# Optimization experiments

Hardware: AMD Instinct MI355X
Metric: run time of the kernel (lower is better)

## Reference

```python
import jax, jax.numpy as jnp
import numpy as np

B, S, DIM = 8, 1024, 192
D2 = 2 * DIM            # inner width 384
CH = 4                  # cell heads (= qk_size)
HD = D2 // CH           # 96 head dim
NB = D2 // 4            # 96 block-diagonal blocks
BLK = D2 // NB          # block size 4
TAU = float(HD) ** 0.5


def setup_inputs() -> dict:
    key = jax.random.key(0)
    ks = jax.random.split(key, 16)
    r = lambda i, shp, s=0.02: jax.random.normal(ks[i], shp, jnp.float32) * s
    return {
        "x": jax.random.normal(ks[0], (B, S, DIM), jnp.float32),
        "ln_g": jnp.ones((DIM,), jnp.float32), "ln_b": jnp.zeros((DIM,), jnp.float32),
        "w1": r(1, (D2, DIM)), "b1": jnp.zeros((D2,), jnp.float32),
        "w2": r(2, (D2, DIM)), "b2": jnp.zeros((D2,), jnp.float32),
        "conv_w": r(3, (D2, 1, 3), 0.1), "conv_b": jnp.zeros((D2,), jnp.float32),
        "qw": r(4, (NB, BLK, BLK), 0.1), "qb": jnp.zeros((D2,), jnp.float32),
        "kw": r(5, (NB, BLK, BLK), 0.1), "kb": jnp.zeros((D2,), jnp.float32),
        "vw": r(6, (NB, BLK, BLK), 0.1), "vb": jnp.zeros((D2,), jnp.float32),
        "wi": r(7, (CH, 3 * D2)), "bi": jax.random.normal(ks[8], (CH,), jnp.float32) * 0.1,
        "wf": r(9, (CH, 3 * D2)), "bf": jnp.linspace(3.0, 6.0, CH).astype(jnp.float32),
        "gn_g": jnp.ones((D2,), jnp.float32), "gn_b": jnp.zeros((D2,), jnp.float32),
        "wo": r(10, (DIM, D2)), "bo": jnp.zeros((DIM,), jnp.float32),
        "skip": jnp.ones((D2,), jnp.float32),
    }


def _layernorm(x, g, b):
    m = x.mean(-1, keepdims=True)
    v = ((x - m) ** 2).mean(-1, keepdims=True)
    return (x - m) / jnp.sqrt(v + 1e-5) * g + b


def _blockdiag(x, w, b):
    # x: [B,S,D2] -> blocks [B,S,NB,BLK]; w: [NB, out_blk, in_blk]
    bs, sq, _ = x.shape
    y = jnp.einsum('bsni,noi->bsno', x.reshape(bs, sq, NB, BLK), w)
    return y.reshape(bs, sq, D2) + b


def _dwconv(x, w, b):
    # depthwise conv over sequence: x [B,S,C] -> [B,C,S] conv -> [B,S,C]
    y = jax.lax.conv_general_dilated(
        x.transpose(0, 2, 1), w, window_strides=(1,), padding=[(1, 1)],
        dimension_numbers=('NCH', 'OIH', 'NCH'), feature_group_count=D2)
    return y.transpose(0, 2, 1) + b


def _cell(q, k, v, wi, bi, wf, bf, gn_g, gn_b):
    bs, sq, _ = q.shape
    gi = jnp.concatenate([q, k, v], axis=-1)                      # [B,S,3*D2]
    it = jnp.einsum('bsc,hc->bhs', gi, wi) + bi[None, :, None]    # [B,H,S]
    ft = jnp.einsum('bsc,hc->bhs', gi, wf) + bf[None, :, None]
    c = jnp.cumsum(jax.nn.log_sigmoid(ft), axis=-1)               # [B,H,S]
    logm = c[..., :, None] - c[..., None, :]                      # cum[i]-cum[j]
    mask = jnp.tril(jnp.ones((sq, sq), dtype=bool))
    f_act = jnp.where(mask, logm, -jnp.inf)
    dt = f_act + it[:, :, None, :]                                # add itilde over cols
    max_d = jnp.max(dt, axis=-1, keepdims=True)
    dmat = jnp.exp(dt - max_d)                                    # [B,H,S,S]
    qh = q.reshape(bs, sq, CH, HD).transpose(0, 2, 1, 3)
    kh = k.reshape(bs, sq, CH, HD).transpose(0, 2, 1, 3)
    vh = v.reshape(bs, sq, CH, HD).transpose(0, 2, 1, 3)
    ct = jnp.einsum('bhid,bhjd->bhij', qh, kh) * dmat / TAU
    maxit = jnp.maximum(jnp.abs(ct.sum(-1, keepdims=True)), jnp.exp(-max_d))
    h = jnp.einsum('bhij,bhjd->bhid', ct, vh) / (maxit + 1e-6)
    h = h.transpose(0, 2, 1, 3).reshape(bs, sq, CH, HD)           # per-token GroupNorm
    mu = h.mean(-1, keepdims=True)
    var = ((h - mu) ** 2).mean(-1, keepdims=True)
    h = (h - mu) / jnp.sqrt(var + 1e-5)
    h = h * gn_g.reshape(CH, HD) + gn_b.reshape(CH, HD)
    return h.reshape(bs, sq, D2)


def reference(x, ln_g, ln_b, w1, b1, w2, b2, conv_w, conv_b, qw, qb, kw, kb,
              vw, vb, wi, bi, wf, bf, gn_g, gn_b, wo, bo, skip):
    inputs = _layernorm(x, ln_g, ln_b)
    a = inputs @ w1.T + b1                   # [B,S,D2]
    bgate = jax.nn.silu(inputs @ w2.T + b2)  # [B,S,D2]
    qk = jax.nn.silu(_dwconv(a, conv_w, conv_b))
    q = _blockdiag(qk, qw, qb)
    k = _blockdiag(qk, kw, kb)
    v = _blockdiag(a, vw, vb)
    out1 = _cell(q, k, v, wi, bi, wf, bf, gn_g, gn_b)
    out1 = (out1 + skip * qk) * bgate
    out = out1 @ wo.T + bo
    return out + x
```

## Files before the change

kernel.cpp:

```cpp
#include <hip/hip_runtime.h>
#include <cstdint>

#define TAU_ 9.797958971132712f

typedef __attribute__((ext_vector_type(4))) float f32x4;
typedef __attribute__((ext_vector_type(8))) short short8;

#define DEV static __device__ __forceinline__

DEV unsigned short f2bf(float f){
  union { float f; unsigned u; } v; v.f = f;
  unsigned r = v.u + 0x7FFFu + ((v.u >> 16) & 1u);
  return (unsigned short)(r >> 16);
}
DEV unsigned pack2bf(float a, float b){
  unsigned r;
  asm("v_cvt_pk_bf16_f32 %0, %1, %2" : "=v"(r) : "v"(a), "v"(b));
  return r;
}
DEV float siluf_(float x){ return x / (1.f + __expf(-x)); }
DEV float logsigf_(float x){ return fminf(x, 0.f) - log1pf(__expf(-fabsf(x))); }

__global__ __launch_bounds__(256) void k01_prep(
    const float* __restrict__ x, const float* __restrict__ ln_g, const float* __restrict__ ln_b,
    const float* __restrict__ w1, const float* __restrict__ w2, const float* __restrict__ wo,
    short* __restrict__ xnbf, short* __restrict__ w12bf, short* __restrict__ wobf)
{
  const int tid = threadIdx.x;
  if(blockIdx.x >= 512){
    int idx = (blockIdx.x - 512) * 256 + tid;
    if(idx < 73728)       w12bf[idx] = (short)f2bf(w1[idx]);
    else if(idx < 147456) w12bf[idx] = (short)f2bf(w2[idx - 73728]);
    else                  wobf[idx - 147456] = (short)f2bf(wo[idx - 147456]);
    return;
  }
  const int t = blockIdx.x * 16 + (tid >> 4);
  const int g = tid & 15;
  const float* xr = x + (long)t * 192 + g * 12;
  f32x4 v0 = *(const f32x4*)(xr);
  f32x4 v1 = *(const f32x4*)(xr + 4);
  f32x4 v2 = *(const f32x4*)(xr + 8);
  float s  = v0[0]+v0[1]+v0[2]+v0[3] + v1[0]+v1[1]+v1[2]+v1[3] + v2[0]+v2[1]+v2[2]+v2[3];
  float sq = v0[0]*v0[0]+v0[1]*v0[1]+v0[2]*v0[2]+v0[3]*v0[3]
           + v1[0]*v1[0]+v1[1]*v1[1]+v1[2]*v1[2]+v1[3]*v1[3]
           + v2[0]*v2[0]+v2[1]*v2[1]+v2[2]*v2[2]+v2[3]*v2[3];
  s  += __shfl_xor(s, 1);  s  += __shfl_xor(s, 2);  s  += __shfl_xor(s, 4);  s  += __shfl_xor(s, 8);
  sq += __shfl_xor(sq, 1); sq += __shfl_xor(sq, 2); sq += __shfl_xor(sq, 4); sq += __shfl_xor(sq, 8);
  const float mean = s * (1.f/192.f);
  const float rstd = rsqrtf(sq * (1.f/192.f) - mean * mean + 1e-5f);
  const int c0 = g * 12;
  f32x4 g0 = *(const f32x4*)(ln_g + c0),     b0 = *(const f32x4*)(ln_b + c0);
  f32x4 g1 = *(const f32x4*)(ln_g + c0 + 4), b1 = *(const f32x4*)(ln_b + c0 + 4);
  f32x4 g2 = *(const f32x4*)(ln_g + c0 + 8), b2 = *(const f32x4*)(ln_b + c0 + 8);
  unsigned pk[6];
  pk[0] = pack2bf((v0[0]-mean)*rstd*g0[0]+b0[0], (v0[1]-mean)*rstd*g0[1]+b0[1]);
  pk[1] = pack2bf((v0[2]-mean)*rstd*g0[2]+b0[2], (v0[3]-mean)*rstd*g0[3]+b0[3]);
  pk[2] = pack2bf((v1[0]-mean)*rstd*g1[0]+b1[0], (v1[1]-mean)*rstd*g1[1]+b1[1]);
  pk[3] = pack2bf((v1[2]-mean)*rstd*g1[2]+b1[2], (v1[3]-mean)*rstd*g1[3]+b1[3]);
  pk[4] = pack2bf((v2[0]-mean)*rstd*g2[0]+b2[0], (v2[1]-mean)*rstd*g2[1]+b2[1]);
  pk[5] = pack2bf((v2[2]-mean)*rstd*g2[2]+b2[2], (v2[3]-mean)*rstd*g2[3]+b2[3]);
  uint2* xo = (uint2*)(xnbf + (long)t * 192 + g * 12);
  xo[0] = make_uint2(pk[0], pk[1]);
  xo[1] = make_uint2(pk[2], pk[3]);
  xo[2] = make_uint2(pk[4], pk[5]);
}

__global__ __launch_bounds__(256) void k1b_gemm(
    const short* __restrict__ xnbf, const short* __restrict__ w12bf,
    const float* __restrict__ b1, const float* __restrict__ b2,
    float* __restrict__ a, float* __restrict__ bgate)
{
  __shared__ short wt[18432];
  const int tid = threadIdx.x;
  const int ntg = blockIdx.x & 7;
  const int t0 = (blockIdx.x >> 3) * 64;
  {
    const short* src = w12bf + (long)ntg * 96 * 192;
    #pragma unroll
    for(int i = 0; i < 9; i++){
      const int u = i * 256 + tid;
      const int row = u / 24;
      const int dst = (u * 16) ^ ((row & 7) << 4);
      *(short8*)((char*)wt + dst) = *(const short8*)(src + u * 8);
    }
  }
  __syncthreads();
  const int widx = tid >> 6, lane = tid & 63, qg = lane >> 4, l16 = lane & 15;
  f32x4 acc[6];
  #pragma unroll
  for(int nt = 0; nt < 6; nt++) acc[nt] = (f32x4){0.f,0.f,0.f,0.f};
  const short* xrow = xnbf + (long)(t0 + widx * 16 + l16) * 192;
  #pragma unroll
  for(int kc = 0; kc < 6; kc++){
    short8 af = *(const short8*)(xrow + kc * 32 + 8 * qg);
    #pragma unroll
    for(int nt = 0; nt < 6; nt++){
      const int row = nt * 16 + l16;
      int byte = row * 384 + (kc * 32 + 8 * qg) * 2;
      byte ^= (row & 7) << 4;
      short8 bfr = *(const short8*)((const char*)wt + byte);
      acc[nt] = __builtin_amdgcn_mfma_f32_16x16x32_bf16(af, bfr, acc[nt], 0, 0, 0);
    }
  }
  const int half = ntg >> 2;
  float* dst = half ? bgate : a;
  const float* bias = half ? b2 : b1;
  const int ncol = (ntg & 3) * 96;
  #pragma unroll
  for(int nt = 0; nt < 6; nt++){
    const int n = ncol + nt * 16 + l16;
    const float bs = bias[n];
    #pragma unroll
    for(int r = 0; r < 4; r++){
      const int trow = t0 + widx * 16 + 4 * qg + r;
      float v = acc[nt][r] + bs;
      if(half) v = siluf_(v);
      dst[(long)trow * 384 + n] = v;
    }
  }
}

__global__ __launch_bounds__(256) void k2bv(
    const float* __restrict__ a, const float* __restrict__ cw, const float* __restrict__ cb,
    const float* __restrict__ qw, const float* __restrict__ qb,
    const float* __restrict__ kw, const float* __restrict__ kb,
    const float* __restrict__ vw, const float* __restrict__ vb,
    float* __restrict__ qkbuf, short* __restrict__ qbf, short* __restrict__ kbf,
    short* __restrict__ vtbf)
{
  __shared__ float vt[64][97];
  const int tid = threadIdx.x;
  const int bh = blockIdx.x >> 4;
  const int b = bh >> 2, h = bh & 3;
  const int s0 = (blockIdx.x & 15) << 6;
  #pragma unroll
  for(int it = 0; it < 6; it++){
    const int f = it * 256 + tid;
    const int sl = f / 24, c4l = f % 24;
    const int c4 = h * 24 + c4l;
    const int s = s0 + sl;
    const long t = (long)b * 1024 + s;
    const long abase = t * 384 + c4 * 4;
    f32x4 am = *(const f32x4*)(a + abase);
    f32x4 al = (s > 0)    ? *(const f32x4*)(a + abase - 384) : (f32x4){0.f,0.f,0.f,0.f};
    f32x4 ar = (s < 1023) ? *(const f32x4*)(a + abase + 384) : (f32x4){0.f,0.f,0.f,0.f};
    f32x4 cw0 = *(const f32x4*)(cw + c4 * 12);
    f32x4 cw1 = *(const f32x4*)(cw + c4 * 12 + 4);
    f32x4 cw2 = *(const f32x4*)(cw + c4 * 12 + 8);
    f32x4 cb4 = *(const f32x4*)(cb + c4 * 4);
    f32x4 in;
    in[0] = siluf_(cb4[0] + al[0]*cw0[0] + am[0]*cw0[1] + ar[0]*cw0[2]);
    in[1] = siluf_(cb4[1] + al[1]*cw0[3] + am[1]*cw1[0] + ar[1]*cw1[1]);
    in[2] = siluf_(cb4[2] + al[2]*cw1[2] + am[2]*cw1[3] + ar[2]*cw2[0]);
    in[3] = siluf_(cb4[3] + al[3]*cw2[1] + am[3]*cw2[2] + ar[3]*cw2[3]);
    *(f32x4*)(qkbuf + abase) = in;
    const long base = ((long)(b * 4 + h) * 1024 + s) * 96 + c4l * 4;
    {
      const float* w = qw + c4 * 16;
      float v0 = qb[c4*4+0] + w[0]*in[0]  + w[1]*in[1]  + w[2]*in[2]  + w[3]*in[3];
      float v1 = qb[c4*4+1] + w[4]*in[0]  + w[5]*in[1]  + w[6]*in[2]  + w[7]*in[3];
      float v2 = qb[c4*4+2] + w[8]*in[0]  + w[9]*in[1]  + w[10]*in[2] + w[11]*in[3];
      float v3 = qb[c4*4+3] + w[12]*in[0] + w[13]*in[1] + w[14]*in[2] + w[15]*in[3];
      uint2 pk; pk.x = pack2bf(v0, v1); pk.y = pack2bf(v2, v3);
      *(uint2*)(qbf + base) = pk;
    }
    {
      const float* w = kw + c4 * 16;
      float v0 = kb[c4*4+0] + w[0]*in[0]  + w[1]*in[1]  + w[2]*in[2]  + w[3]*in[3];
      float v1 = kb[c4*4+1] + w[4]*in[0]  + w[5]*in[1]  + w[6]*in[2]  + w[7]*in[3];
      float v2 = kb[c4*4+2] + w[8]*in[0]  + w[9]*in[1]  + w[10]*in[2] + w[11]*in[3];
      float v3 = kb[c4*4+3] + w[12]*in[0] + w[13]*in[1] + w[14]*in[2] + w[15]*in[3];
      uint2 pk; pk.x = pack2bf(v0, v1); pk.y = pack2bf(v2, v3);
      *(uint2*)(kbf + base) = pk;
    }
    {
      const float* w = vw + c4 * 16;
      #pragma unroll
      for(int o = 0; o < 4; o++){
        float v = vb[c4*4+o] + w[o*4]*am[0] + w[o*4+1]*am[1] + w[o*4+2]*am[2] + w[o*4+3]*am[3];
        vt[sl][c4l * 4 + o] = v;
      }
    }
  }
  __syncthreads();
  #pragma unroll
  for(int it = 0; it < 24; it++){
    const int f = it * 256 + tid;
    const int d = f >> 6, sl = f & 63;
    vtbf[((long)bh * 96 + d) * 1024 + s0 + sl] = (short)f2bf(vt[sl][d]);
  }
}

__global__ __launch_bounds__(256) void k2c_gates(
    const float* __restrict__ qk, const float* __restrict__ a,
    const float* __restrict__ qw, const float* __restrict__ qb,
    const float* __restrict__ kw, const float* __restrict__ kb,
    const float* __restrict__ vw, const float* __restrict__ vb,
    const float* __restrict__ wi, const float* __restrict__ bi,
    const float* __restrict__ wf, const float* __restrict__ bff,
    float* __restrict__ itv, float* __restrict__ ftv)
{
  const int tid = threadIdx.x;
  const int lane = tid & 63, widx = tid >> 6;
  const int t = blockIdx.x * 4 + widx;
  const int b = t >> 10, s = t & 1023;
  float pit[4] = {0,0,0,0}, pft[4] = {0,0,0,0};
  for(int j = 0; j < 18; j++){
    const int e = lane + 64 * j;
    float val;
    if(e < 768){
      const int c = (e >= 384) ? e - 384 : e;
      const int c4 = c >> 2, o = c & 3;
      const float* W  = (e >= 384) ? kw : qw;
      const float* Bv = (e >= 384) ? kb : qb;
      f32x4 in = *(const f32x4*)(qk + (long)t * 384 + c4 * 4);
      const float* w = W + c4 * 16 + o * 4;
      val = Bv[c] + w[0]*in[0] + w[1]*in[1] + w[2]*in[2] + w[3]*in[3];
    } else {
      const int c = e - 768;
      const int c4 = c >> 2, o = c & 3;
      f32x4 in = *(const f32x4*)(a + (long)t * 384 + c4 * 4);
      const float* w = vw + c4 * 16 + o * 4;
      val = vb[c] + w[0]*in[0] + w[1]*in[1] + w[2]*in[2] + w[3]*in[3];
    }
    #pragma unroll
    for(int h = 0; h < 4; h++){
      pit[h] += val * wi[h * 1152 + e];
      pft[h] += val * wf[h * 1152 + e];
    }
  }
  #pragma unroll
  for(int h = 0; h < 4; h++){
    float vi = pit[h], vf = pft[h];
    #pragma unroll
    for(int m = 1; m < 64; m <<= 1){ vi += __shfl_xor(vi, m); vf += __shfl_xor(vf, m); }
    if(lane == 0){
      itv[((long)(b * 4 + h)) * 1024 + s] = vi + bi[h];
      ftv[((long)(b * 4 + h)) * 1024 + s] = vf + bff[h];
    }
  }
}

__global__ __launch_bounds__(256) void k3_scan(
    const float* __restrict__ itv, const float* __restrict__ ftv,
    float* __restrict__ Ev, float* __restrict__ Rpv, float* __restrict__ dsv)
{
  __shared__ float sb[256];
  const int bh = blockIdx.x, tid = threadIdx.x;
  const long base = (long)bh * 1024 + tid * 4;
  f32x4 f4 = *(const f32x4*)(ftv + base);
  const float l0 = logsigf_(f4[0]);
  const float l1 = logsigf_(f4[1]);
  const float l2 = logsigf_(f4[2]);
  const float l3 = logsigf_(f4[3]);
  float c0 = l0, c1 = l0 + l1, c2 = c1 + l2, c3 = c2 + l3;
  sb[tid] = c3;
  __syncthreads();
  for(int off = 1; off < 256; off <<= 1){
    float mine = sb[tid];
    float oth = (tid >= off) ? sb[tid - off] : 0.f;
    __syncthreads();
    sb[tid] = mine + oth;
    __syncthreads();
  }
  const float excl = (tid > 0) ? sb[tid - 1] : 0.f;
  c0 += excl; c1 += excl; c2 += excl; c3 += excl;
  f32x4 i4 = *(const f32x4*)(itv + base);
  const float m0 = i4[0] - c0, m1 = i4[1] - c1, m2 = i4[2] - c2, m3 = i4[3] - c3;
  const float x1 = fmaxf(m0, m1), x2 = fmaxf(x1, m2), x3 = fmaxf(x2, m3);
  __syncthreads();
  sb[tid] = x3;
  __syncthreads();
  for(int off = 1; off < 256; off <<= 1){
    float mine = sb[tid];
    float oth = (tid >= off) ? sb[tid - off] : -3.4e38f;
    __syncthreads();
    sb[tid] = fmaxf(mine, oth);
    __syncthreads();
  }
  const float exm = (tid > 0) ? sb[tid - 1] : -3.4e38f;
  const float M0 = fmaxf(m0, exm);
  const float M1 = fmaxf(x1, exm);
  const float M2 = fmaxf(x2, exm);
  const float M3 = fmaxf(x3, exm);
  f32x4 e, rp, ds;
  e[0] = __expf(m0); e[1] = __expf(m1); e[2] = __expf(m2); e[3] = __expf(m3);
  rp[0] = __expf(-M0) * (1.f/TAU_); rp[1] = __expf(-M1) * (1.f/TAU_);
  rp[2] = __expf(-M2) * (1.f/TAU_); rp[3] = __expf(-M3) * (1.f/TAU_);
  ds[0] = __expf(-(c0 + M0)); ds[1] = __expf(-(c1 + M1));
  ds[2] = __expf(-(c2 + M2)); ds[3] = __expf(-(c3 + M3));
  *(f32x4*)(Ev  + base) = e;
  *(f32x4*)(Rpv + base) = rp;
  *(f32x4*)(dsv + base) = ds;
}

__global__ __launch_bounds__(256, 2) void k4_attn(
    const short* __restrict__ qbf, const short* __restrict__ kbf, const short* __restrict__ vtbf,
    const float* __restrict__ Ev, const float* __restrict__ Rpv, const float* __restrict__ dsv,
    const float* __restrict__ gn_g, const float* __restrict__ gn_b,
    const float* __restrict__ qk, const float* __restrict__ bgate, const float* __restrict__ skip,
    short* __restrict__ o1bf)
{
  __shared__ short kbuf[2][64 * 104];
  __shared__ short vbuf[2][96 * 72];
  __shared__ float ebuf[2][64];
  __shared__ short P[4][16][72];
  const int tid = threadIdx.x;
  const int w = tid >> 6, lane = tid & 63, qg = lane >> 4, l16 = lane & 15;
  const int xcd = blockIdx.x & 7, q = blockIdx.x >> 3;
  const int bh = ((q & 3) << 3) | xcd;
  const int qh = q >> 2;
  const int ib = (q < 32) ? (15 - qh) : (qh - 8);
  const int i0w = ib * 64 + w * 16;
  const long qkbase = (long)bh * 1024;
  const int nj = ib + 1;

  short8 qf[3];
  #pragma unroll
  for(int kc = 0; kc < 3; kc++)
    qf[kc] = *(const short8*)(qbf + (qkbase + i0w + l16) * 96 + kc * 32 + 8 * qg);
  const float rp = Rpv[qkbase + i0w + l16];
  const float ds = dsv[qkbase + i0w + l16];

  f32x4 acc[6];
  #pragma unroll
  for(int dt = 0; dt < 6; dt++) acc[dt] = (f32x4){0.f,0.f,0.f,0.f};
  float bp = 0.f;

  const int rK0 = tid / 12,        cK0 = tid % 12;
  const int rK1 = (tid+256) / 12,  cK1 = (tid+256) % 12;
  const int rK2 = (tid+512) / 12,  cK2 = (tid+512) % 12;
  const int dV0 = tid >> 3,        cV0 = tid & 7;
  const int dV1 = (tid+256) >> 3,  cV1 = (tid+256) & 7;
  const int dV2 = (tid+512) >> 3,  cV2 = (tid+512) & 7;
  const bool he = (tid < 16);
  short8 sk0, sk1, sk2, sv0, sv1, sv2; f32x4 se;
  const short* kgb = kbf + qkbase * 96;
  const short* vgb = vtbf + (long)bh * 96 * 1024;

#define STAGE_LOAD(J0)                                              \
  {                                                                 \
    const int j0_ = (J0);                                           \
    sk0 = *(const short8*)(kgb + (j0_ + rK0) * 96 + cK0 * 8);       \
    sk1 = *(const short8*)(kgb + (j0_ + rK1) * 96 + cK1 * 8);       \
    sk2 = *(const short8*)(kgb + (j0_ + rK2) * 96 + cK2 * 8);       \
    sv0 = *(const short8*)(vgb + (long)dV0 * 1024 + j0_ + cV0 * 8); \
    sv1 = *(const short8*)(vgb + (long)dV1 * 1024 + j0_ + cV1 * 8); \
    sv2 = *(const short8*)(vgb + (long)dV2 * 1024 + j0_ + cV2 * 8); \
    if(he) se = *(const f32x4*)(Ev + qkbase + j0_ + tid * 4);       \
  }

#define STAGE_WRITE(B)                                   \
  {                                                      \
    *(short8*)(&kbuf[B][rK0 * 104 + cK0 * 8]) = sk0;     \
    *(short8*)(&kbuf[B][rK1 * 104 + cK1 * 8]) = sk1;     \
    *(short8*)(&kbuf[B][rK2 * 104 + cK2 * 8]) = sk2;     \
    *(short8*)(&vbuf[B][dV0 * 72 + cV0 * 8]) = sv0;      \
    *(short8*)(&vbuf[B][dV1 * 72 + cV1 * 8]) = sv1;      \
    *(short8*)(&vbuf[B][dV2 * 72 + cV2 * 8]) = sv2;      \
    if(he) *(f32x4*)(&ebuf[B][tid * 4]) = se;            \
  }

  STAGE_LOAD(0);
  int cur = 0;
  for(int jt = 0; jt < nj; jt++){
    STAGE_WRITE(cur);
    __syncthreads();
    if(jt + 1 < nj) STAGE_LOAD((jt + 1) * 64);

    const int j0 = jt * 64;
    const bool diag = (jt == nj - 1);
    const int i = i0w + l16;
    __builtin_amdgcn_s_setprio(1);
    #pragma unroll
    for(int jsub = 0; jsub < 4; jsub++){
      f32x4 C = (f32x4){0.f,0.f,0.f,0.f};
      #pragma unroll
      for(int kc = 0; kc < 3; kc++){
        short8 kf = *(const short8*)(&kbuf[cur][(jsub*16 + l16) * 104 + kc * 32 + 8 * qg]);
        C = __builtin_amdgcn_mfma_f32_16x16x32_bf16(kf, qf[kc], C, 0, 0, 0);
      }
      f32x4 e4 = *(const f32x4*)(&ebuf[cur][jsub * 16 + 4 * qg]);
      float v0 = C[0] * e4[0];
      float v1 = C[1] * e4[1];
      float v2 = C[2] * e4[2];
      float v3 = C[3] * e4[3];
      if(diag){
        const int jb = j0 + jsub * 16 + 4 * qg;
        if(jb + 0 > i) v0 = 0.f;
        if(jb + 1 > i) v1 = 0.f;
        if(jb + 2 > i) v2 = 0.f;
        if(jb + 3 > i) v3 = 0.f;
      }
      bp += v0 + v1 + v2 + v3;
      uint2 pw; pw.x = pack2bf(v0, v1); pw.y = pack2bf(v2, v3);
      *(uint2*)(&P[w][l16][jsub * 16 + 4 * qg]) = pw;
    }
    asm volatile("s_waitcnt lgkmcnt(0)" ::: "memory");
    #pragma unroll
    for(int ksub = 0; ksub < 2; ksub++){
      short8 pa = *(const short8*)(&P[w][l16][ksub * 32 + 8 * qg]);
      #pragma unroll
      for(int dt = 0; dt < 6; dt++){
        short8 vf = *(const short8*)(&vbuf[cur][(dt * 16 + l16) * 72 + ksub * 32 + 8 * qg]);
        acc[dt] = __builtin_amdgcn_mfma_f32_16x16x32_bf16(pa, vf, acc[dt], 0, 0, 0);
      }
    }
    __builtin_amdgcn_s_setprio(0);
    cur ^= 1;
  }
#undef STAGE_LOAD
#undef STAGE_WRITE

  const int head = bh & 3, bb = bh >> 2;
  float bsum = bp;
  bsum += __shfl_xor(bsum, 16);
  bsum += __shfl_xor(bsum, 32);
  const float bfull = bsum * rp;
  const float den = fmaxf(fabsf(bfull), ds) + 1e-6f;
  const float sc = rp / den;
  float srow[4];
  #pragma unroll
  for(int r = 0; r < 4; r++) srow[r] = __shfl(sc, 4 * qg + r);
  float hv[6][4], mu[4], rs[4];
  #pragma unroll
  for(int r = 0; r < 4; r++){
    float sm = 0.f, sq = 0.f;
    #pragma unroll
    for(int dt = 0; dt < 6; dt++){
      const float h = acc[dt][r] * srow[r];
      hv[dt][r] = h; sm += h; sq += h * h;
    }
    sm += __shfl_xor(sm, 1); sm += __shfl_xor(sm, 2); sm += __shfl_xor(sm, 4); sm += __shfl_xor(sm, 8);
    sq += __shfl_xor(sq, 1); sq += __shfl_xor(sq, 2); sq += __shfl_xor(sq, 4); sq += __shfl_xor(sq, 8);
    const float m_ = sm * (1.f/96.f);
    mu[r] = m_;
    rs[r] = rsqrtf(sq * (1.f/96.f) - m_ * m_ + 1e-5f);
  }
  #pragma unroll
  for(int dt = 0; dt < 6; dt++){
    const int col = head * 96 + dt * 16 + l16;
    const float g  = gn_g[col];
    const float be = gn_b[col];
    const float sk = skip[col];
    #pragma unroll
    for(int r = 0; r < 4; r++){
      const long off = ((long)(bb * 1024 + i0w + 4 * qg + r)) * 384 + col;
      const float hn = (hv[dt][r] - mu[r]) * rs[r] * g + be;
      const float o1 = (hn + sk * qk[off]) * bgate[off];
      o1bf[off] = (short)f2bf(o1);
    }
  }
}

__global__ __launch_bounds__(256) void k5_gemm(
    const short* __restrict__ o1bf, const short* __restrict__ wobf,
    const float* __restrict__ bo, const float* __restrict__ x, float* __restrict__ out)
{
  __shared__ short wt[18432];
  const int tid = threadIdx.x;
  const int ng = blockIdx.x & 3;
  const int t0 = (blockIdx.x >> 2) * 64;
  {
    const short* src = wobf + (long)ng * 48 * 384;
    #pragma unroll
    for(int i = 0; i < 9; i++){
      const int u = i * 256 + tid;
      const int row = u / 48;
      const int dst = (u * 16) ^ ((row & 7) << 4);
      *(short8*)((char*)wt + dst) = *(const short8*)(src + u * 8);
    }
  }
  __syncthreads();
  const int widx = tid >> 6, lane = tid & 63, qg = lane >> 4, l16 = lane & 15;
  f32x4 acc[3];
  #pragma unroll
  for(int nt = 0; nt < 3; nt++) acc[nt] = (f32x4){0.f,0.f,0.f,0.f};
  const short* arow = o1bf + (long)(t0 + widx * 16 + l16) * 384;
  #pragma unroll
  for(int kc = 0; kc < 12; kc++){
    short8 af = *(const short8*)(arow + kc * 32 + 8 * qg);
    #pragma unroll
    for(int nt = 0; nt < 3; nt++){
      const int row = nt * 16 + l16;
      int byte = row * 768 + kc * 64 + qg * 16;
      byte ^= (row & 7) << 4;
      short8 bfr = *(const short8*)((const char*)wt + byte);
      acc[nt] = __builtin_amdgcn_mfma_f32_16x16x32_bf16(af, bfr, acc[nt], 0, 0, 0);
    }
  }
  #pragma unroll
  for(int nt = 0; nt < 3; nt++){
    const int n = ng * 48 + nt * 16 + l16;
    const float b_ = bo[n];
    #pragma unroll
    for(int r = 0; r < 4; r++){
      const int trow = t0 + widx * 16 + 4 * qg + r;
      out[(long)trow * 192 + n] = acc[nt][r] + b_ + x[(long)trow * 192 + n];
    }
  }
}

extern "C" void kernel_launch(void* const* d_in, const int* in_sizes, int n_in,
                              void* d_out, int out_size, void* d_ws, size_t ws_size,
                              hipStream_t stream)
{
  (void)in_sizes; (void)n_in; (void)out_size; (void)ws_size;
  const float* x    = (const float*)d_in[0];
  const float* ln_g = (const float*)d_in[1];
  const float* ln_b = (const float*)d_in[2];
  const float* w1   = (const float*)d_in[3];
  const float* b1   = (const float*)d_in[4];
  const float* w2   = (const float*)d_in[5];
  const float* b2   = (const float*)d_in[6];
  const float* cw   = (const float*)d_in[7];
  const float* cb   = (const float*)d_in[8];
  const float* qw   = (const float*)d_in[9];
  const float* qb   = (const float*)d_in[10];
  const float* kw   = (const float*)d_in[11];
  const float* kb   = (const float*)d_in[12];
  const float* vw   = (const float*)d_in[13];
  const float* vb   = (const float*)d_in[14];
  const float* wi   = (const float*)d_in[15];
  const float* bi   = (const float*)d_in[16];
  const float* wf   = (const float*)d_in[17];
  const float* bff  = (const float*)d_in[18];
  const float* gn_g = (const float*)d_in[19];
  const float* gn_b = (const float*)d_in[20];
  const float* wo   = (const float*)d_in[21];
  const float* bo   = (const float*)d_in[22];
  const float* skip = (const float*)d_in[23];
  float* out = (float*)d_out;

  char* ws = (char*)d_ws;
  float* a_    = (float*)(ws + 0);
  float* bgate = (float*)(ws + 12582912);
  float* qkbuf = (float*)(ws + 25165824);
  short* xnbf  = (short*)(ws + 37748736);
  short* o1bf  = (short*)(ws + 41943040);
  short* qbf   = (short*)(ws + 50331648);
  short* kbf   = (short*)(ws + 56623104);
  short* vtbf  = (short*)(ws + 62914560);
  short* w12bf = (short*)(ws + 69206016);
  short* wobf  = (short*)(ws + 69500928);
  float* itv   = (float*)(ws + 69648384);
  float* ftv   = (float*)(ws + 69779456);
  float* Ev    = (float*)(ws + 69910528);
  float* Rpv   = (float*)(ws + 70041600);
  float* dsv   = (float*)(ws + 70172672);

  k01_prep<<<1376, 256, 0, stream>>>(x, ln_g, ln_b, w1, w2, wo, xnbf, w12bf, wobf);
  k1b_gemm<<<1024, 256, 0, stream>>>(xnbf, w12bf, b1, b2, a_, bgate);
  k2bv<<<512, 256, 0, stream>>>(a_, cw, cb, qw, qb, kw, kb, vw, vb, qkbuf, qbf, kbf, vtbf);
  k2c_gates<<<2048, 256, 0, stream>>>(qkbuf, a_, qw, qb, kw, kb, vw, vb, wi, bi, wf, bff, itv, ftv);
  k3_scan<<<32, 256, 0, stream>>>(itv, ftv, Ev, Rpv, dsv);
  k4_attn<<<512, 256, 0, stream>>>(qbf, kbf, vtbf, Ev, Rpv, dsv, gn_g, gn_b,
                                   qkbuf, bgate, skip, o1bf);
  k5_gemm<<<512, 256, 0, stream>>>(o1bf, wobf, bo, x, out);
}
```

Baseline: 90.72 us.

## Fuse LayerNorm and weight conversion into GEMMs; store gate in bf16, reuse q/k bf16

Removes the separate prep kernel by computing LayerNorm in the first GEMM's prologue into shared memory and converting fp32 weights to bf16 while loading them into LDS in both GEMMs. The bgate activation is stored as bf16, halving its write and read traffic, and the gate kernel reads the already-computed bf16 q/k instead of recomputing the block-diagonal projections. In exchange, each GEMM block redoes the weight conversion and LayerNorm work (redundant across the 8 column groups). Gate inputs and bgate also lose precision by going through bf16.

```diff
diff --git a/kernel.cpp b/kernel.cpp
--- a/kernel.cpp
+++ b/kernel.cpp
@@ -13,6 +13,9 @@
   unsigned r = v.u + 0x7FFFu + ((v.u >> 16) & 1u);
   return (unsigned short)(r >> 16);
 }
+DEV float bf2f(unsigned short u){
+  union { unsigned u; float f; } v; v.u = ((unsigned)u) << 16; return v.f;
+}
 DEV unsigned pack2bf(float a, float b){
   unsigned r;
   asm("v_cvt_pk_bf16_f32 %0, %1, %2" : "=v"(r) : "v"(a), "v"(b));
@@ -21,78 +24,66 @@
 DEV float siluf_(float x){ return x / (1.f + __expf(-x)); }
 DEV float logsigf_(float x){ return fminf(x, 0.f) - log1pf(__expf(-fabsf(x))); }
 
-__global__ __launch_bounds__(256) void k01_prep(
+__global__ __launch_bounds__(256) void k1b_gemm(
     const float* __restrict__ x, const float* __restrict__ ln_g, const float* __restrict__ ln_b,
-    const float* __restrict__ w1, const float* __restrict__ w2, const float* __restrict__ wo,
-    short* __restrict__ xnbf, short* __restrict__ w12bf, short* __restrict__ wobf)
-{
-  const int tid = threadIdx.x;
-  if(blockIdx.x >= 512){
-    int idx = (blockIdx.x - 512) * 256 + tid;
-    if(idx < 73728)       w12bf[idx] = (short)f2bf(w1[idx]);
-    else if(idx < 147456) w12bf[idx] = (short)f2bf(w2[idx - 73728]);
-    else                  wobf[idx - 147456] = (short)f2bf(wo[idx - 147456]);
-    return;
-  }
-  const int t = blockIdx.x * 16 + (tid >> 4);
-  const int g = tid & 15;
-  const float* xr = x + (long)t * 192 + g * 12;
-  f32x4 v0 = *(const f32x4*)(xr);
-  f32x4 v1 = *(const f32x4*)(xr + 4);
-  f32x4 v2 = *(const f32x4*)(xr + 8);
-  float s  = v0[0]+v0[1]+v0[2]+v0[3] + v1[0]+v1[1]+v1[2]+v1[3] + v2[0]+v2[1]+v2[2]+v2[3];
-  float sq = v0[0]*v0[0]+v0[1]*v0[1]+v0[2]*v0[2]+v0[3]*v0[3]
-           + v1[0]*v1[0]+v1[1]*v1[1]+v1[2]*v1[2]+v1[3]*v1[3]
-           + v2[0]*v2[0]+v2[1]*v2[1]+v2[2]*v2[2]+v2[3]*v2[3];
-  s  += __shfl_xor(s, 1);  s  += __shfl_xor(s, 2);  s  += __shfl_xor(s, 4);  s  += __shfl_xor(s, 8);
-  sq += __shfl_xor(sq, 1); sq += __shfl_xor(sq, 2); sq += __shfl_xor(sq, 4); sq += __shfl_xor(sq, 8);
-  const float mean = s * (1.f/192.f);
-  const float rstd = rsqrtf(sq * (1.f/192.f) - mean * mean + 1e-5f);
-  const int c0 = g * 12;
-  f32x4 g0 = *(const f32x4*)(ln_g + c0),     b0 = *(const f32x4*)(ln_b + c0);
-  f32x4 g1 = *(const f32x4*)(ln_g + c0 + 4), b1 = *(const f32x4*)(ln_b + c0 + 4);
-  f32x4 g2 = *(const f32x4*)(ln_g + c0 + 8), b2 = *(const f32x4*)(ln_b + c0 + 8);
-  unsigned pk[6];
-  pk[0] = pack2bf((v0[0]-mean)*rstd*g0[0]+b0[0], (v0[1]-mean)*rstd*g0[1]+b0[1]);
-  pk[1] = pack2bf((v0[2]-mean)*rstd*g0[2]+b0[2], (v0[3]-mean)*rstd*g0[3]+b0[3]);
-  pk[2] = pack2bf((v1[0]-mean)*rstd*g1[0]+b1[0], (v1[1]-mean)*rstd*g1[1]+b1[1]);
-  pk[3] = pack2bf((v1[2]-mean)*rstd*g1[2]+b1[2], (v1[3]-mean)*rstd*g1[3]+b1[3]);
-  pk[4] = pack2bf((v2[0]-mean)*rstd*g2[0]+b2[0], (v2[1]-mean)*rstd*g2[1]+b2[1]);
-  pk[5] = pack2bf((v2[2]-mean)*rstd*g2[2]+b2[2], (v2[3]-mean)*rstd*g2[3]+b2[3]);
-  uint2* xo = (uint2*)(xnbf + (long)t * 192 + g * 12);
-  xo[0] = make_uint2(pk[0], pk[1]);
-  xo[1] = make_uint2(pk[2], pk[3]);
-  xo[2] = make_uint2(pk[4], pk[5]);
-}
-
-__global__ __launch_bounds__(256) void k1b_gemm(
-    const short* __restrict__ xnbf, const short* __restrict__ w12bf,
+    const float* __restrict__ w1, const float* __restrict__ w2,
     const float* __restrict__ b1, const float* __restrict__ b2,
-    float* __restrict__ a, float* __restrict__ bgate)
-{
+    float* __restrict__ a, unsigned short* __restrict__ bgate)
+{
+  __shared__ short xn[64][200];
   __shared__ short wt[18432];
   const int tid = threadIdx.x;
   const int ntg = blockIdx.x & 7;
   const int t0 = (blockIdx.x >> 3) * 64;
   {
-    const short* src = w12bf + (long)ntg * 96 * 192;
+    const int row = tid >> 2, g = tid & 3;
+    const float* xr = x + (long)(t0 + row) * 192 + g * 48;
+    float xv[48];
+    float s = 0.f, sq = 0.f;
+    #pragma unroll
+    for(int i = 0; i < 12; i++){
+      f32x4 v = *(const f32x4*)(xr + i * 4);
+      xv[i*4+0]=v[0]; xv[i*4+1]=v[1]; xv[i*4+2]=v[2]; xv[i*4+3]=v[3];
+      s  += v[0]+v[1]+v[2]+v[3];
+      sq += v[0]*v[0]+v[1]*v[1]+v[2]*v[2]+v[3]*v[3];
+    }
+    s  += __shfl_xor(s, 1);  s  += __shfl_xor(s, 2);
+    sq += __shfl_xor(sq, 1); sq += __shfl_xor(sq, 2);
+    const float mean = s * (1.f/192.f);
+    const float rstd = rsqrtf(sq * (1.f/192.f) - mean * mean + 1e-5f);
+    unsigned* xrow = (unsigned*)&xn[row][0];
+    #pragma unroll
+    for(int i = 0; i < 48; i += 2){
+      const int c = g * 48 + i;
+      float v0 = (xv[i]   - mean) * rstd * ln_g[c]   + ln_b[c];
+      float v1 = (xv[i+1] - mean) * rstd * ln_g[c+1] + ln_b[c+1];
+      xrow[c >> 1] = pack2bf(v0, v1);
+    }
+  }
+  {
+    const float* src = (ntg < 4 ? w1 : w2) + (long)(ntg & 3) * 96 * 192;
     #pragma unroll
     for(int i = 0; i < 9; i++){
       const int u = i * 256 + tid;
       const int row = u / 24;
       const int dst = (u * 16) ^ ((row & 7) << 4);
-      *(short8*)((char*)wt + dst) = *(const short8*)(src + u * 8);
+      f32x4 f0 = *(const f32x4*)(src + u * 8);
+      f32x4 f1 = *(const f32x4*)(src + u * 8 + 4);
+      uint4 pk;
+      pk.x = pack2bf(f0[0], f0[1]); pk.y = pack2bf(f0[2], f0[3]);
+      pk.z = pack2bf(f1[0], f1[1]); pk.w = pack2bf(f1[2], f1[3]);
+      *(uint4*)((char*)wt + dst) = pk;
     }
   }
   __syncthreads();
   const int widx = tid >> 6, lane = tid & 63, qg = lane >> 4, l16 = lane & 15;
+  const int mrow = widx * 16 + l16;
   f32x4 acc[6];
   #pragma unroll
   for(int nt = 0; nt < 6; nt++) acc[nt] = (f32x4){0.f,0.f,0.f,0.f};
-  const short* xrow = xnbf + (long)(t0 + widx * 16 + l16) * 192;
   #pragma unroll
   for(int kc = 0; kc < 6; kc++){
-    short8 af = *(const short8*)(xrow + kc * 32 + 8 * qg);
+    short8 af = *(const short8*)(&xn[mrow][0] + kc * 32 + 8 * qg);
     #pragma unroll
     for(int nt = 0; nt < 6; nt++){
       const int row = nt * 16 + l16;
@@ -103,7 +94,6 @@
     }
   }
   const int half = ntg >> 2;
-  float* dst = half ? bgate : a;
   const float* bias = half ? b2 : b1;
   const int ncol = (ntg & 3) * 96;
   #pragma unroll
@@ -114,8 +104,8 @@
     for(int r = 0; r < 4; r++){
       const int trow = t0 + widx * 16 + 4 * qg + r;
       float v = acc[nt][r] + bs;
-      if(half) v = siluf_(v);
-      dst[(long)trow * 384 + n] = v;
+      if(half) bgate[(long)trow * 384 + n] = f2bf(siluf_(v));
+      else     a[(long)trow * 384 + n] = v;
     }
   }
 }
@@ -192,9 +182,8 @@
 }
 
 __global__ __launch_bounds__(256) void k2c_gates(
-    const float* __restrict__ qk, const float* __restrict__ a,
-    const float* __restrict__ qw, const float* __restrict__ qb,
-    const float* __restrict__ kw, const float* __restrict__ kb,
+    const short* __restrict__ qbf, const short* __restrict__ kbf,
+    const float* __restrict__ a,
     const float* __restrict__ vw, const float* __restrict__ vb,
     const float* __restrict__ wi, const float* __restrict__ bi,
     const float* __restrict__ wf, const float* __restrict__ bff,
@@ -210,12 +199,9 @@
     float val;
     if(e < 768){
       const int c = (e >= 384) ? e - 384 : e;
-      const int c4 = c >> 2, o = c & 3;
-      const float* W  = (e >= 384) ? kw : qw;
-      const float* Bv = (e >= 384) ? kb : qb;
-      f32x4 in = *(const f32x4*)(qk + (long)t * 384 + c4 * 4);
-      const float* w = W + c4 * 16 + o * 4;
-      val = Bv[c] + w[0]*in[0] + w[1]*in[1] + w[2]*in[2] + w[3]*in[3];
+      const short* src = (e >= 384) ? kbf : qbf;
+      const int h = c / 96, d = c - h * 96;
+      val = bf2f((unsigned short)src[((long)(b * 4 + h) * 1024 + s) * 96 + d]);
     } else {
       const int c = e - 768;
       const int c4 = c >> 2, o = c & 3;
@@ -298,8 +284,8 @@
     const short* __restrict__ qbf, const short* __restrict__ kbf, const short* __restrict__ vtbf,
     const float* __restrict__ Ev, const float* __restrict__ Rpv, const float* __restrict__ dsv,
     const float* __restrict__ gn_g, const float* __restrict__ gn_b,
-    const float* __restrict__ qk, const float* __restrict__ bgate, const float* __restrict__ skip,
-    short* __restrict__ o1bf)
+    const float* __restrict__ qk, const unsigned short* __restrict__ bgate,
+    const float* __restrict__ skip, short* __restrict__ o1bf)
 {
   __shared__ short kbuf[2][64 * 104];
   __shared__ short vbuf[2][96 * 72];
@@ -447,14 +433,14 @@
     for(int r = 0; r < 4; r++){
       const long off = ((long)(bb * 1024 + i0w + 4 * qg + r)) * 384 + col;
       const float hn = (hv[dt][r] - mu[r]) * rs[r] * g + be;
-      const float o1 = (hn + sk * qk[off]) * bgate[off];
+      const float o1 = (hn + sk * qk[off]) * bf2f(bgate[off]);
       o1bf[off] = (short)f2bf(o1);
     }
   }
 }
 
 __global__ __launch_bounds__(256) void k5_gemm(
-    const short* __restrict__ o1bf, const short* __restrict__ wobf,
+    const short* __restrict__ o1bf, const float* __restrict__ wo,
     const float* __restrict__ bo, const float* __restrict__ x, float* __restrict__ out)
 {
   __shared__ short wt[18432];
@@ -462,13 +448,18 @@
   const int ng = blockIdx.x & 3;
   const int t0 = (blockIdx.x >> 2) * 64;
   {
-    const short* src = wobf + (long)ng * 48 * 384;
+    const float* src = wo + (long)ng * 48 * 384;
     #pragma unroll
     for(int i = 0; i < 9; i++){
       const int u = i * 256 + tid;
       const int row = u / 48;
       const int dst = (u * 16) ^ ((row & 7) << 4);
-      *(short8*)((char*)wt + dst) = *(const short8*)(src + u * 8);
+      f32x4 f0 = *(const f32x4*)(src + u * 8);
+      f32x4 f1 = *(const f32x4*)(src + u * 8 + 4);
+      uint4 pk;
+      pk.x = pack2bf(f0[0], f0[1]); pk.y = pack2bf(f0[2], f0[3]);
+      pk.z = pack2bf(f1[0], f1[1]); pk.w = pack2bf(f1[2], f1[3]);
+      *(uint4*)((char*)wt + dst) = pk;
     }
   }
   __syncthreads();
@@ -534,27 +525,23 @@
 
   char* ws = (char*)d_ws;
   float* a_    = (float*)(ws + 0);
-  float* bgate = (float*)(ws + 12582912);
+  unsigned short* bgate = (unsigned short*)(ws + 12582912);
   float* qkbuf = (float*)(ws + 25165824);
-  short* xnbf  = (short*)(ws + 37748736);
   short* o1bf  = (short*)(ws + 41943040);
   short* qbf   = (short*)(ws + 50331648);
   short* kbf   = (short*)(ws + 56623104);
   short* vtbf  = (short*)(ws + 62914560);
-  short* w12bf = (short*)(ws + 69206016);
-  short* wobf  = (short*)(ws + 69500928);
   float* itv   = (float*)(ws + 69648384);
   float* ftv   = (float*)(ws + 69779456);
   float* Ev    = (float*)(ws + 69910528);
   float* Rpv   = (float*)(ws + 70041600);
   float* dsv   = (float*)(ws + 70172672);
 
-  k01_prep<<<1376, 256, 0, stream>>>(x, ln_g, ln_b, w1, w2, wo, xnbf, w12bf, wobf);
-  k1b_gemm<<<1024, 256, 0, stream>>>(xnbf, w12bf, b1, b2, a_, bgate);
+  k1b_gemm<<<1024, 256, 0, stream>>>(x, ln_g, ln_b, w1, w2, b1, b2, a_, bgate);
   k2bv<<<512, 256, 0, stream>>>(a_, cw, cb, qw, qb, kw, kb, vw, vb, qkbuf, qbf, kbf, vtbf);
-  k2c_gates<<<2048, 256, 0, stream>>>(qkbuf, a_, qw, qb, kw, kb, vw, vb, wi, bi, wf, bff, itv, ftv);
+  k2c_gates<<<2048, 256, 0, stream>>>(qbf, kbf, a_, vw, vb, wi, bi, wf, bff, itv, ftv);
   k3_scan<<<32, 256, 0, stream>>>(itv, ftv, Ev, Rpv, dsv);
   k4_attn<<<512, 256, 0, stream>>>(qbf, kbf, vtbf, Ev, Rpv, dsv, gn_g, gn_b,
                                    qkbuf, bgate, skip, o1bf);
-  k5_gemm<<<512, 256, 0, stream>>>(o1bf, wobf, bo, x, out);
-}
+  k5_gemm<<<512, 256, 0, stream>>>(o1bf, wo, bo, x, out);
+}
```

After: 92.36 us. Within noise of the previous version (+1.8%).
